# Performance work log

Hardware: AMD Instinct MI355X
Metric: run time of the kernel (lower is better)

Reference implementation:

```python
import jax, jax.numpy as jnp
import numpy as np
import math

D_MODEL = 768
HEADS = 12
D_FF = 3072
B, S = 2, 2048


def layer_norm(x, g, b, eps=1e-6):
    mu = jnp.mean(x, axis=-1, keepdims=True)
    var = jnp.mean((x - mu) ** 2, axis=-1, keepdims=True)
    return (x - mu) / jnp.sqrt(var + eps) * g + b


def gelu_tanh(x):
    c = math.sqrt(2.0 / math.pi)
    return 0.5 * x * (1.0 + jnp.tanh(c * (x + 0.044715 * x ** 3)))


def setup_inputs() -> dict:
    key = jax.random.key(0)
    ks = jax.random.split(key, 12)
    s = 0.02
    inp = {
        "iter": 1,
        "query": jax.random.normal(ks[0], (B, S, D_MODEL), jnp.float32),
        "inputs": jax.random.normal(ks[1], (B, S, D_MODEL), jnp.float32),
        "mask": jax.random.randint(ks[2], (B, S), 0, 2).astype(bool),
        "Wq": jax.random.normal(ks[3], (D_MODEL, D_MODEL), jnp.float32) * s,
        "bq": jnp.zeros((D_MODEL,), jnp.float32),
        "Wk": jax.random.normal(ks[4], (D_MODEL, D_MODEL), jnp.float32) * s,
        "bk": jnp.zeros((D_MODEL,), jnp.float32),
        "Wv": jax.random.normal(ks[5], (D_MODEL, D_MODEL), jnp.float32) * s,
        "bv": jnp.zeros((D_MODEL,), jnp.float32),
        "Wo": jax.random.normal(ks[6], (D_MODEL, D_MODEL), jnp.float32) * s,
        "bo": jnp.zeros((D_MODEL,), jnp.float32),
        "ln1_g": jnp.ones((D_MODEL,), jnp.float32),
        "ln1_b": jnp.zeros((D_MODEL,), jnp.float32),
        "W1": jax.random.normal(ks[7], (D_MODEL, D_FF), jnp.float32) * s,
        "b1": jnp.zeros((D_FF,), jnp.float32),
        "W2": jax.random.normal(ks[8], (D_FF, D_MODEL), jnp.float32) * s,
        "b2": jnp.zeros((D_MODEL,), jnp.float32),
        "ln2_g": jnp.ones((D_MODEL,), jnp.float32),
        "ln2_b": jnp.zeros((D_MODEL,), jnp.float32),
    }
    return inp


def reference(iter, query, inputs, mask, Wq, bq, Wk, bk, Wv, bv, Wo, bo,
              ln1_g, ln1_b, W1, b1, W2, b2, ln2_g, ln2_b):
    dh = D_MODEL // HEADS
    # pre-LN (skipped when iter == 0)
    x = layer_norm(inputs, ln1_g, ln1_b) if iter != 0 else inputs
    # QKV projections -> [B, H, S, dh]
    def heads(t):
        return t.reshape(B, S, HEADS, dh).transpose(0, 2, 1, 3)
    q = heads(x @ Wq + bq) / math.sqrt(dh)
    k = heads(x @ Wk + bk)
    v = heads(x @ Wv + bv)
    scores = jnp.einsum("bhqd,bhkd->bhqk", q, k)
    scores = jnp.where(mask[:, None, None, :], -1e18, scores)
    attn = jax.nn.softmax(scores, axis=-1)
    ctx = jnp.einsum("bhqk,bhkd->bhqd", attn, v)
    ctx = ctx.transpose(0, 2, 1, 3).reshape(B, S, D_MODEL)
    attn_out = ctx @ Wo + bo
    out = attn_out + inputs  # dropout=0 -> identity
    # FFN with residual pre-LN and tanh-GELU
    h = layer_norm(out, ln2_g, ln2_b)
    inter = gelu_tanh(h @ W1 + b1)
    return inter @ W2 + b2 + out
```

## Files before the change

### kernel.cpp

```cpp
#include <hip/hip_runtime.h>
#include <hip/hip_bf16.h>
#include <stdint.h>

#define D_MODEL 768
#define HEADS   12
#define DHEAD   64
#define D_FF    3072
#define BB      2
#define SS      2048
#define MTOT    (BB*SS)

typedef uint16_t u16;
typedef uint32_t u32;
typedef __attribute__((ext_vector_type(8))) short short8;
typedef __attribute__((ext_vector_type(4))) short short4v;
typedef __attribute__((ext_vector_type(4))) float f32x4;
typedef __attribute__((ext_vector_type(16))) float f32x16;
typedef __attribute__((ext_vector_type(2))) unsigned uint2v;

__device__ __forceinline__ u16 f2bf(float f) {
    union { float f; u32 u; } v; v.f = f;
    u32 r = v.u + 0x7fffu + ((v.u >> 16) & 1u);
    return (u16)(r >> 16);
}

__device__ __forceinline__ float bf2f(u16 u) {
    union { u32 u; float f; } v; v.u = ((u32)u) << 16;
    return v.f;
}

__device__ __forceinline__ u32 cvtpk(float a, float b) {
    u32 r;
    asm("v_cvt_pk_bf16_f32 %0, %1, %2" : "=v"(r) : "v"(a), "v"(b));
    return r;
}

__device__ __forceinline__ void plswap(u32& a, u32& b, int hi) {
#if __has_builtin(__builtin_amdgcn_permlane32_swap)
    uint2v r = __builtin_amdgcn_permlane32_swap(a, b, false, false);
    a = r[0]; b = r[1];
#else
    u32 ax = (u32)__shfl_xor((int)a, 32), bx = (u32)__shfl_xor((int)b, 32);
    u32 na = hi ? bx : a, nb = hi ? b : ax;
    a = na; b = nb;
#endif
}

__device__ __forceinline__ void gload16(const void* g, void* l) {
    __builtin_amdgcn_global_load_lds(
        (const __attribute__((address_space(1))) u32*)g,
        (__attribute__((address_space(3))) u32*)l, 16, 0, 0);
}

#define MFMA16(a, b, c) __builtin_amdgcn_mfma_f32_16x16x32_bf16((a), (b), (c), 0, 0, 0)
#define MFMA32(a, b, c) __builtin_amdgcn_mfma_f32_32x32x16_bf16((a), (b), (c), 0, 0, 0)

__device__ __forceinline__ float gelu_tanh_f(float x) {
    float x3 = x * x * x;
    return 0.5f * x * (1.0f + tanhf(0.7978845608028654f * (x + 0.044715f * x3)));
}

__global__ __launch_bounds__(256)
void transpose_cast(const float* __restrict__ W, u16* __restrict__ Wt, int R, int C) {
    __shared__ float tile[32][33];
    int bx = blockIdx.x, by = blockIdx.y;
    int x = threadIdx.x & 31, y0 = threadIdx.x >> 5;
#pragma unroll
    for (int i = 0; i < 4; ++i) {
        int y = y0 + i * 8;
        tile[y][x] = W[(size_t)(by * 32 + y) * C + bx * 32 + x];
    }
    __syncthreads();
#pragma unroll
    for (int i = 0; i < 4; ++i) {
        int y = y0 + i * 8;
        Wt[(size_t)(bx * 32 + y) * R + by * 32 + x] = f2bf(tile[x][y]);
    }
}

__global__ __launch_bounds__(256)
void transpose_cast4(const float* __restrict__ W0, const float* __restrict__ W1,
                     const float* __restrict__ W2, const float* __restrict__ W3,
                     u16* __restrict__ T0, u16* __restrict__ T1,
                     u16* __restrict__ T2, u16* __restrict__ T3) {
    const int z = blockIdx.z;
    const float* W = z == 0 ? W0 : z == 1 ? W1 : z == 2 ? W2 : W3;
    u16*         T = z == 0 ? T0 : z == 1 ? T1 : z == 2 ? T2 : T3;
    __shared__ float tile[32][33];
    int bx = blockIdx.x, by = blockIdx.y;
    int x = threadIdx.x & 31, y0 = threadIdx.x >> 5;
#pragma unroll
    for (int i = 0; i < 4; ++i) {
        int y = y0 + i * 8;
        tile[y][x] = W[(size_t)(by * 32 + y) * 768 + bx * 32 + x];
    }
    __syncthreads();
#pragma unroll
    for (int i = 0; i < 4; ++i) {
        int y = y0 + i * 8;
        T[(size_t)(bx * 32 + y) * 768 + by * 32 + x] = f2bf(tile[x][y]);
    }
}

__global__ void maskprep(const int* __restrict__ m, float* __restrict__ vz,
                         u16* __restrict__ m01, int n) {
    int i = blockIdx.x * 256 + threadIdx.x;
    if (i < n) {
        float v = m[i] ? 0.0f : 1.0f;
        vz[i] = v;
        m01[i] = f2bf(v);
    }
}

__global__ __launch_bounds__(256)
void ln_bf16(const float* __restrict__ in, const float* __restrict__ g,
             const float* __restrict__ bta, u16* __restrict__ out,
             const int* __restrict__ iterp, int checkIter) {
    int row = blockIdx.x, tid = threadIdx.x;
    const float* x = in + (size_t)row * D_MODEL;
    float v0 = x[tid], v1 = x[tid + 256], v2 = x[tid + 512];
    float s = v0 + v1 + v2;
    float s2 = v0 * v0 + v1 * v1 + v2 * v2;
#pragma unroll
    for (int o = 1; o < 64; o <<= 1) { s += __shfl_xor(s, o); s2 += __shfl_xor(s2, o); }
    __shared__ float sh[8];
    int w = tid >> 6;
    if ((tid & 63) == 0) { sh[w] = s; sh[4 + w] = s2; }
    __syncthreads();
    s = sh[0] + sh[1] + sh[2] + sh[3];
    s2 = sh[4] + sh[5] + sh[6] + sh[7];
    float mu = s * (1.0f / 768.0f);
    float var = s2 * (1.0f / 768.0f) - mu * mu;
    float rstd = rsqrtf(var + 1e-6f);
    bool skip = checkIter && (iterp[0] == 0);
    u16* o0 = out + (size_t)row * D_MODEL;
    if (skip) {
        o0[tid] = f2bf(v0); o0[tid + 256] = f2bf(v1); o0[tid + 512] = f2bf(v2);
    } else {
        o0[tid]       = f2bf((v0 - mu) * rstd * g[tid]       + bta[tid]);
        o0[tid + 256] = f2bf((v1 - mu) * rstd * g[tid + 256] + bta[tid + 256]);
        o0[tid + 512] = f2bf((v2 - mu) * rstd * g[tid + 512] + bta[tid + 512]);
    }
}

__global__ __launch_bounds__(256)
void ln_fuse(const float* __restrict__ pf, const float* __restrict__ bias,
             const float* __restrict__ res, const float* __restrict__ g,
             const float* __restrict__ bta, float* __restrict__ outm,
             u16* __restrict__ out) {
    int row = blockIdx.x, tid = threadIdx.x;
    size_t i0 = (size_t)row * D_MODEL + tid;
    const float* pf1 = pf + (size_t)MTOT * D_MODEL;
    float v0 = pf[i0]       + pf1[i0]       + bias[tid]       + res[i0];
    float v1 = pf[i0 + 256] + pf1[i0 + 256] + bias[tid + 256] + res[i0 + 256];
    float v2 = pf[i0 + 512] + pf1[i0 + 512] + bias[tid + 512] + res[i0 + 512];
    outm[i0] = v0; outm[i0 + 256] = v1; outm[i0 + 512] = v2;
    float s = v0 + v1 + v2;
    float s2 = v0 * v0 + v1 * v1 + v2 * v2;
#pragma unroll
    for (int o = 1; o < 64; o <<= 1) { s += __shfl_xor(s, o); s2 += __shfl_xor(s2, o); }
    __shared__ float sh[8];
    int w = tid >> 6;
    if ((tid & 63) == 0) { sh[w] = s; sh[4 + w] = s2; }
    __syncthreads();
    s = sh[0] + sh[1] + sh[2] + sh[3];
    s2 = sh[4] + sh[5] + sh[6] + sh[7];
    float mu = s * (1.0f / 768.0f);
    float var = s2 * (1.0f / 768.0f) - mu * mu;
    float rstd = rsqrtf(var + 1e-6f);
    u16* o0 = out + (size_t)row * D_MODEL;
    o0[tid]       = f2bf((v0 - mu) * rstd * g[tid]       + bta[tid]);
    o0[tid + 256] = f2bf((v1 - mu) * rstd * g[tid + 256] + bta[tid + 256]);
    o0[tid + 512] = f2bf((v2 - mu) * rstd * g[tid + 512] + bta[tid + 512]);
}

template <int MODE>
__global__ __launch_bounds__(256, 3)
void gemm_bt(const u16* __restrict__ A, const u16* __restrict__ Bt,
             int K, int N,
             const float* __restrict__ bias0, const float* __restrict__ bias1,
             const float* __restrict__ bias2,
             const float* __restrict__ res,
             float* __restrict__ outF, u16* __restrict__ oq,
             u16* __restrict__ ok, u16* __restrict__ ov) {
    __shared__ __align__(16) u16 aT[3][128 * 32];
    __shared__ __align__(16) u16 bT[3][128 * 32];
    const int tid = threadIdx.x;
    const int lane = tid & 63;
    const int w = tid >> 6;
    const int wr = w >> 1, wc = w & 1;
    const int lm = lane & 15, lq = lane >> 4;
    const int bm = blockIdx.y, bn = blockIdx.x;
    const int kzlen = K / gridDim.z;
    const int kbeg = blockIdx.z * kzlen;
    const int nsteps = kzlen >> 5;

    const u16* Abase = A  + (size_t)(bm * 128) * K + kbeg;
    const u16* Bbase = Bt + (size_t)(bn * 128) * K + kbeg;

    auto stage = [&](int buf, int t) {
        int k0 = t * 32;
#pragma unroll
        for (int j = 0; j < 2; ++j) {
            int d = j * 256 + tid;
            int row = d >> 2, p = d & 3;
            int src = (p ^ (row & 3)) * 8;
            gload16(Abase + (size_t)row * K + k0 + src, aT[buf] + (j * 256 + w * 64) * 8);
            gload16(Bbase + (size_t)row * K + k0 + src, bT[buf] + (j * 256 + w * 64) * 8);
        }
    };

    f32x4 acc[4][4] = {};
    stage(0, 0);
    if (nsteps > 1) stage(1, 1);

#pragma unroll 1
    for (int t = 0; t < nsteps; ++t) {
        if (t + 1 < nsteps) asm volatile("s_waitcnt vmcnt(4)" ::: "memory");
        else                asm volatile("s_waitcnt vmcnt(0)" ::: "memory");
        __syncthreads();
        const u16* Ab = aT[t % 3];
        const u16* Bb = bT[t % 3];
        short8 av[4], bv[4];
#pragma unroll
        for (int m = 0; m < 4; ++m) {
            int row = wr * 64 + m * 16 + lm;
            av[m] = *(const short8*)(Ab + row * 32 + ((lq ^ (row & 3)) * 8));
        }
#pragma unroll
        for (int n = 0; n < 4; ++n) {
            int row = wc * 64 + n * 16 + lm;
            bv[n] = *(const short8*)(Bb + row * 32 + ((lq ^ (row & 3)) * 8));
        }
#pragma unroll
        for (int m = 0; m < 4; ++m)
#pragma unroll
            for (int n = 0; n < 4; ++n)
                acc[m][n] = MFMA16(av[m], bv[n], acc[m][n]);
        if (t + 2 < nsteps) stage((t + 2) % 3, t + 2);
    }

#pragma unroll
    for (int m = 0; m < 4; ++m) {
#pragma unroll
        for (int n = 0; n < 4; ++n) {
            int col = bn * 128 + wc * 64 + n * 16 + lm;
#pragma unroll
            for (int r = 0; r < 4; ++r) {
                int row = bm * 128 + wr * 64 + m * 16 + lq * 4 + r;
                float v = acc[m][n][r];
                if (MODE == 0) {
                    int proj = col / D_MODEL;
                    int d = col - proj * D_MODEL;
                    int hh = d >> 6, dhi = d & 63;
                    int bb = row >> 11, sIdx = row & 2047;
                    if (proj == 0) {
                        v = (v + bias0[d]) * 0.18033688011112042f;
                        oq[((size_t)(bb * HEADS + hh) * SS + sIdx) * DHEAD + dhi] = f2bf(v);
                    } else if (proj == 1) {
                        v = v + bias1[d];
                        ok[((size_t)(bb * HEADS + hh) * SS + sIdx) * DHEAD + dhi] = f2bf(v);
                    } else {
                        v = (v + bias2[d]) * res[row];
                        ov[((size_t)(bb * HEADS + hh) * DHEAD + dhi) * SS + sIdx] = f2bf(v);
                    }
                } else if (MODE == 1) {
                    if (gridDim.z > 1) {
                        outF[((size_t)blockIdx.z * MTOT + row) * N + col] = v;
                    } else {
                        size_t idx = (size_t)row * N + col;
                        outF[idx] = v + bias0[col] + res[idx];
                    }
                } else {
                    float t2 = v + bias0[col];
                    oq[(size_t)row * N + col] = f2bf(gelu_tanh_f(t2));
                }
            }
        }
    }
}

__global__ __launch_bounds__(256)
void reduce_ks2(const float* __restrict__ pf, const float* __restrict__ bias,
                const float* __restrict__ res, float* __restrict__ out, int N) {
    size_t i = ((size_t)blockIdx.x * 256 + threadIdx.x) * 4;
    f32x4 s0 = *(const f32x4*)(pf + i);
    f32x4 s1 = *(const f32x4*)(pf + (size_t)MTOT * N + i);
    int col = (int)(i % (size_t)N);
    f32x4 b = *(const f32x4*)(bias + col);
    f32x4 r = *(const f32x4*)(res + i);
    f32x4 o;
#pragma unroll
    for (int e = 0; e < 4; ++e) o[e] = s0[e] + s1[e] + b[e] + r[e];
    *(f32x4*)(out + i) = o;
}

template <int NCH>
__global__ __launch_bounds__(256, 4)
void attn_fwd4(const u16* __restrict__ q, const u16* __restrict__ k,
               const u16* __restrict__ vtg, const u16* __restrict__ m01g,
               u16* __restrict__ po, float* __restrict__ pml) {
    constexpr int KLEN = SS / NCH;
    constexpr int KT   = KLEN / 64;
    __shared__ __align__(16) u16 kls[2][64 * 64];
    __shared__ __align__(16) u16 vls[2][64 * 64];
    __shared__ __align__(16) u16 m01l[KLEN];

    const int tid = threadIdx.x, lane = tid & 63, w = tid >> 6;
    const int lm = lane & 31, hi = lane >> 5;
    const int head = blockIdx.y;
    const int qblk = blockIdx.x / NCH, chunk = blockIdx.x % NCH;
    const int q0 = qblk * 128;
    const int k0 = chunk * KLEN;

    const u16* qbase = q + (size_t)head * SS * DHEAD;
    const u16* kbase = k + (size_t)head * SS * DHEAD;
    const u16* vbase = vtg + (size_t)head * DHEAD * SS;
    const u16* m01row = m01g + (head / HEADS) * SS;

    short8 qf[4];
    const int qrow = q0 + w * 32 + lm;
#pragma unroll
    for (int c = 0; c < 4; ++c)
        qf[c] = *(const short8*)(qbase + (size_t)qrow * DHEAD + c * 16 + hi * 8);

    if (tid < KLEN / 8)
        gload16(m01row + k0 + (size_t)tid * 8, m01l + (size_t)w * 64 * 8);

    auto stage = [&](int buf, int t) {
#pragma unroll
        for (int j = 0; j < 2; ++j) {
            int c = j * 256 + tid;
            int row = c >> 3, jj = c & 7;
            gload16(kbase + (size_t)(k0 + t * 64 + row) * DHEAD + ((jj ^ (row & 7)) * 8),
                    kls[buf] + (j * 256 + w * 64) * 8);
            gload16(vbase + (size_t)row * SS + k0 + t * 64 + ((jj ^ (row & 7)) * 8),
                    vls[buf] + (j * 256 + w * 64) * 8);
        }
    };
    stage(0, 0);
    asm volatile("s_waitcnt vmcnt(0)" ::: "memory");
    __syncthreads();

    f32x16 o0 = {}, o1 = {}, accl = {};
    int cur = 0;

#pragma unroll 1
    for (int t = 0; t < KT; ++t) {
        if (t < KT - 1) stage(cur ^ 1, t + 1);
        const u16* kb = kls[cur];
        const u16* vb = vls[cur];
#pragma unroll
        for (int s = 0; s < 2; ++s) {
            short8 av[4];
#pragma unroll
            for (int c = 0; c < 4; ++c)
                av[c] = *(const short8*)(kb + (s * 32 + lm) * 64 + (((c * 2 + hi) ^ (lm & 7)) * 8));
            short8 vf[4];
#pragma unroll
            for (int kc = 0; kc < 2; ++kc)
#pragma unroll
                for (int df = 0; df < 2; ++df)
                    vf[kc * 2 + df] = *(const short8*)(vb + (df * 32 + lm) * 64 +
                                                       (((s * 4 + kc * 2 + hi) ^ (lm & 7)) * 8));
            short8 mf0 = *(const short8*)(m01l + t * 64 + s * 32 + hi * 8);
            short8 mf1 = *(const short8*)(m01l + t * 64 + s * 32 + 16 + hi * 8);

            f32x16 st = {};
#pragma unroll
            for (int c = 0; c < 4; ++c) st = MFMA32(av[c], qf[c], st);

            float p[16];
#pragma unroll
            for (int r = 0; r < 16; ++r) p[r] = exp2f(st[r]);

            u32 W[8];
#pragma unroll
            for (int t8 = 0; t8 < 8; ++t8) W[t8] = cvtpk(p[2 * t8], p[2 * t8 + 1]);
            union { u32 wd[4]; short8 s8; } pf0, pf1;
            u32 a0w = W[0], b0w = W[2]; plswap(a0w, b0w, hi);
            u32 a1w = W[1], b1w = W[3]; plswap(a1w, b1w, hi);
            u32 a2w = W[4], b2w = W[6]; plswap(a2w, b2w, hi);
            u32 a3w = W[5], b3w = W[7]; plswap(a3w, b3w, hi);
            pf0.wd[0] = a0w; pf0.wd[1] = a1w; pf0.wd[2] = b0w; pf0.wd[3] = b1w;
            pf1.wd[0] = a2w; pf1.wd[1] = a3w; pf1.wd[2] = b2w; pf1.wd[3] = b3w;

            accl = MFMA32(mf0, pf0.s8, accl);
            accl = MFMA32(mf1, pf1.s8, accl);
            o0 = MFMA32(vf[0], pf0.s8, o0);
            o1 = MFMA32(vf[1], pf0.s8, o1);
            o0 = MFMA32(vf[2], pf1.s8, o0);
            o1 = MFMA32(vf[3], pf1.s8, o1);
        }
        asm volatile("s_waitcnt vmcnt(0)" ::: "memory");
        __syncthreads();
        cur ^= 1;
    }

    const int pc = (head * 16 + qblk) * NCH + chunk;
    u16* orow = po + ((size_t)pc * 128 + (w * 32 + lm)) * 64;
#pragma unroll
    for (int g = 0; g < 4; ++g) {
        short4v pk0, pk1;
#pragma unroll
        for (int e = 0; e < 4; ++e) {
            pk0[e] = (short)f2bf(o0[g * 4 + e]);
            pk1[e] = (short)f2bf(o1[g * 4 + e]);
        }
        *(short4v*)(orow + g * 8 + hi * 4) = pk0;
        *(short4v*)(orow + 32 + g * 8 + hi * 4) = pk1;
    }
    if (hi == 0)
        pml[(size_t)pc * 128 + (w * 32 + lm)] = accl[0];
}

__global__ __launch_bounds__(256)
void attn_merge(const u16* __restrict__ po, const float* __restrict__ pml,
                u16* __restrict__ ctx, int nch) {
    const int head = blockIdx.y;
    const int bb = head / HEADS, hh = head % HEADS;
    const int rl = threadIdx.x >> 4, dg = threadIdx.x & 15;
    const int s = blockIdx.x * 16 + rl;
    const int qb = s >> 7, qr = s & 127;
    const int pcb = (head * 16 + qb) * nch;

    float denom = 0.0f;
    float acc[4] = {0.0f, 0.0f, 0.0f, 0.0f};
#pragma unroll 4
    for (int c = 0; c < nch; ++c) {
        denom += pml[((size_t)(pcb + c)) * 128 + qr];
        const u16* op = po + (((size_t)(pcb + c) * 128 + qr) * 64) + dg * 4;
        short4v a = *(const short4v*)op;
#pragma unroll
        for (int e = 0; e < 4; ++e) acc[e] += bf2f((u16)a[e]);
    }
    float inv = 1.0f / denom;
    short4v r;
#pragma unroll
    for (int e = 0; e < 4; ++e) r[e] = (short)f2bf(acc[e] * inv);
    *(short4v*)(ctx + ((size_t)(bb * SS + s)) * D_MODEL + hh * DHEAD + dg * 4) = r;
}

extern "C" void kernel_launch(void* const* d_in, const int* in_sizes, int n_in,
                              void* d_out, int out_size, void* d_ws, size_t ws_size,
                              hipStream_t stream) {
    const int*   iterp  = (const int*)  d_in[0];
    const float* inputs = (const float*)d_in[2];
    const int*   mask   = (const int*)  d_in[3];
    const float* Wq = (const float*)d_in[4];
    const float* bq = (const float*)d_in[5];
    const float* Wk = (const float*)d_in[6];
    const float* bk = (const float*)d_in[7];
    const float* Wv = (const float*)d_in[8];
    const float* bv = (const float*)d_in[9];
    const float* Wo = (const float*)d_in[10];
    const float* bo = (const float*)d_in[11];
    const float* ln1g = (const float*)d_in[12];
    const float* ln1b = (const float*)d_in[13];
    const float* W1 = (const float*)d_in[14];
    const float* b1 = (const float*)d_in[15];
    const float* W2 = (const float*)d_in[16];
    const float* b2 = (const float*)d_in[17];
    const float* ln2g = (const float*)d_in[18];
    const float* ln2b = (const float*)d_in[19];
    float* outp = (float*)d_out;

    char* ws = (char*)d_ws;
    size_t off = 0;
    auto alloc = [&](size_t bytes) -> void* {
        void* p = ws + off;
        off += (bytes + 255) & ~(size_t)255;
        return p;
    };
    u16*   wqkv_t = (u16*)  alloc((size_t)2304 * 768 * 2);
    u16*   wo_t   = (u16*)  alloc((size_t)768 * 768 * 2);
    u16*   w1_t   = (u16*)  alloc((size_t)3072 * 768 * 2);
    u16*   w2_t   = (u16*)  alloc((size_t)768 * 3072 * 2);
    float* vzf    = (float*)alloc((size_t)MTOT * 4);
    u16*   m01    = (u16*)  alloc((size_t)MTOT * 2);
    u16*   xh     = (u16*)  alloc((size_t)MTOT * 768 * 2);
    u16*   qb     = (u16*)  alloc((size_t)MTOT * 768 * 2);
    u16*   kbuf   = (u16*)  alloc((size_t)MTOT * 768 * 2);
    u16*   vtb    = (u16*)  alloc((size_t)MTOT * 768 * 2);
    u16*   ctxb   = (u16*)  alloc((size_t)MTOT * 768 * 2);
    float* outm   = (float*)alloc((size_t)MTOT * 768 * 4);
    u16*   inter  = qb;

    float* pfbuf = (float*)alloc((size_t)2 * MTOT * 768 * 4);
    const bool split_ok = (off <= ws_size);

    float* pml = (float*)xh;

    dim3 blk(256);
    transpose_cast4<<<dim3(24, 24, 4), blk, 0, stream>>>(
        Wq, Wk, Wv, Wo,
        wqkv_t, wqkv_t + 768 * 768, wqkv_t + 2 * 768 * 768, wo_t);
    transpose_cast<<<dim3(96, 24), blk, 0, stream>>>(W1, w1_t, 768, 3072);
    transpose_cast<<<dim3(24, 96), blk, 0, stream>>>(W2, w2_t, 3072, 768);
    maskprep<<<dim3(16), blk, 0, stream>>>(mask, vzf, m01, MTOT);

    ln_bf16<<<dim3(MTOT), blk, 0, stream>>>(inputs, ln1g, ln1b, xh, iterp, 1);

    gemm_bt<0><<<dim3(2304 / 128, MTOT / 128), blk, 0, stream>>>(
        xh, wqkv_t, 768, 2304, bq, bk, bv, vzf, nullptr, qb, kbuf, vtb);

    if (split_ok) {
        u16* po = (u16*)pfbuf;
        attn_fwd4<4><<<dim3(16 * 4, BB * HEADS), blk, 0, stream>>>(
            qb, kbuf, vtb, m01, po, pml);
        attn_merge<<<dim3(SS / 16, BB * HEADS), blk, 0, stream>>>(po, pml, ctxb, 4);
    } else {
        u16* po = (u16*)outm;
        attn_fwd4<2><<<dim3(16 * 2, BB * HEADS), blk, 0, stream>>>(
            qb, kbuf, vtb, m01, po, pml);
        attn_merge<<<dim3(SS / 16, BB * HEADS), blk, 0, stream>>>(po, pml, ctxb, 2);
    }

    if (split_ok) {
        gemm_bt<1><<<dim3(768 / 128, MTOT / 128, 2), blk, 0, stream>>>(
            ctxb, wo_t, 768, 768, nullptr, nullptr, nullptr, nullptr,
            pfbuf, nullptr, nullptr, nullptr);
        ln_fuse<<<dim3(MTOT), blk, 0, stream>>>(pfbuf, bo, inputs, ln2g, ln2b, outm, xh);
    } else {
        gemm_bt<1><<<dim3(768 / 128, MTOT / 128), blk, 0, stream>>>(
            ctxb, wo_t, 768, 768, bo, nullptr, nullptr, inputs, outm, nullptr, nullptr, nullptr);
        ln_bf16<<<dim3(MTOT), blk, 0, stream>>>(outm, ln2g, ln2b, xh, iterp, 0);
    }

    gemm_bt<2><<<dim3(3072 / 128, MTOT / 128), blk, 0, stream>>>(
        xh, w1_t, 768, 3072, b1, nullptr, nullptr, nullptr, nullptr, inter, nullptr, nullptr);

    if (split_ok) {
        gemm_bt<1><<<dim3(768 / 128, MTOT / 128, 2), blk, 0, stream>>>(
            inter, w2_t, 3072, 768, nullptr, nullptr, nullptr, nullptr,
            pfbuf, nullptr, nullptr, nullptr);
        reduce_ks2<<<dim3(MTOT * 768 / 1024), blk, 0, stream>>>(pfbuf, b2, outm, outp, 768);
    } else {
        gemm_bt<1><<<dim3(768 / 128, MTOT / 128), blk, 0, stream>>>(
            inter, w2_t, 3072, 768, b2, nullptr, nullptr, outm, outp, nullptr, nullptr, nullptr);
    }
}
```

Before: 229.9 us.

## Widen attention blocks to 512 threads with triple-buffered K/V staging and MFMA priority

The attention kernel now uses 512-thread blocks covering 256 query rows, so each staged K/V tile is shared by twice as many waves. It triple-buffers K/V in LDS and issues loads two tiles ahead, waiting with a partial vmcnt instead of draining all loads each iteration. MFMA sections are wrapped in s_setprio to favour matrix issue over the exp and pack work. The grid halves, which lowers block count and raises LDS use per block, and the merge kernel's indexing is updated to match.

```diff
diff --git a/kernel.cpp b/kernel.cpp
--- a/kernel.cpp
+++ b/kernel.cpp
@@ -296,21 +296,21 @@
 }
 
 template <int NCH>
-__global__ __launch_bounds__(256, 4)
-void attn_fwd4(const u16* __restrict__ q, const u16* __restrict__ k,
+__global__ __launch_bounds__(512, 6)
+void attn_fwd5(const u16* __restrict__ q, const u16* __restrict__ k,
                const u16* __restrict__ vtg, const u16* __restrict__ m01g,
                u16* __restrict__ po, float* __restrict__ pml) {
     constexpr int KLEN = SS / NCH;
     constexpr int KT   = KLEN / 64;
-    __shared__ __align__(16) u16 kls[2][64 * 64];
-    __shared__ __align__(16) u16 vls[2][64 * 64];
+    __shared__ __align__(16) u16 kls[3][64 * 64];
+    __shared__ __align__(16) u16 vls[3][64 * 64];
     __shared__ __align__(16) u16 m01l[KLEN];
 
     const int tid = threadIdx.x, lane = tid & 63, w = tid >> 6;
     const int lm = lane & 31, hi = lane >> 5;
     const int head = blockIdx.y;
     const int qblk = blockIdx.x / NCH, chunk = blockIdx.x % NCH;
-    const int q0 = qblk * 128;
+    const int q0 = qblk * 256;
     const int k0 = chunk * KLEN;
 
     const u16* qbase = q + (size_t)head * SS * DHEAD;
@@ -325,31 +325,27 @@
         qf[c] = *(const short8*)(qbase + (size_t)qrow * DHEAD + c * 16 + hi * 8);
 
     if (tid < KLEN / 8)
-        gload16(m01row + k0 + (size_t)tid * 8, m01l + (size_t)w * 64 * 8);
+        gload16(m01row + k0 + (size_t)tid * 8, m01l + (size_t)(tid >> 6) * 64 * 8);
 
     auto stage = [&](int buf, int t) {
-#pragma unroll
-        for (int j = 0; j < 2; ++j) {
-            int c = j * 256 + tid;
-            int row = c >> 3, jj = c & 7;
-            gload16(kbase + (size_t)(k0 + t * 64 + row) * DHEAD + ((jj ^ (row & 7)) * 8),
-                    kls[buf] + (j * 256 + w * 64) * 8);
-            gload16(vbase + (size_t)row * SS + k0 + t * 64 + ((jj ^ (row & 7)) * 8),
-                    vls[buf] + (j * 256 + w * 64) * 8);
-        }
+        int row = tid >> 3, jj = tid & 7;
+        gload16(kbase + (size_t)(k0 + t * 64 + row) * DHEAD + ((jj ^ (row & 7)) * 8),
+                kls[buf] + (size_t)w * 64 * 8);
+        gload16(vbase + (size_t)row * SS + k0 + t * 64 + ((jj ^ (row & 7)) * 8),
+                vls[buf] + (size_t)w * 64 * 8);
     };
     stage(0, 0);
-    asm volatile("s_waitcnt vmcnt(0)" ::: "memory");
-    __syncthreads();
+    if (KT > 1) stage(1, 1);
 
     f32x16 o0 = {}, o1 = {}, accl = {};
-    int cur = 0;
 
 #pragma unroll 1
     for (int t = 0; t < KT; ++t) {
-        if (t < KT - 1) stage(cur ^ 1, t + 1);
-        const u16* kb = kls[cur];
-        const u16* vb = vls[cur];
+        if (t + 1 < KT) asm volatile("s_waitcnt vmcnt(2)" ::: "memory");
+        else            asm volatile("s_waitcnt vmcnt(0)" ::: "memory");
+        __syncthreads();
+        const u16* kb = kls[t % 3];
+        const u16* vb = vls[t % 3];
 #pragma unroll
         for (int s = 0; s < 2; ++s) {
             short8 av[4];
@@ -367,8 +363,10 @@
             short8 mf1 = *(const short8*)(m01l + t * 64 + s * 32 + 16 + hi * 8);
 
             f32x16 st = {};
+            __builtin_amdgcn_s_setprio(1);
 #pragma unroll
             for (int c = 0; c < 4; ++c) st = MFMA32(av[c], qf[c], st);
+            __builtin_amdgcn_s_setprio(0);
 
             float p[16];
 #pragma unroll
@@ -385,20 +383,20 @@
             pf0.wd[0] = a0w; pf0.wd[1] = a1w; pf0.wd[2] = b0w; pf0.wd[3] = b1w;
             pf1.wd[0] = a2w; pf1.wd[1] = a3w; pf1.wd[2] = b2w; pf1.wd[3] = b3w;
 
+            __builtin_amdgcn_s_setprio(1);
             accl = MFMA32(mf0, pf0.s8, accl);
             accl = MFMA32(mf1, pf1.s8, accl);
             o0 = MFMA32(vf[0], pf0.s8, o0);
             o1 = MFMA32(vf[1], pf0.s8, o1);
             o0 = MFMA32(vf[2], pf1.s8, o0);
             o1 = MFMA32(vf[3], pf1.s8, o1);
+            __builtin_amdgcn_s_setprio(0);
         }
-        asm volatile("s_waitcnt vmcnt(0)" ::: "memory");
-        __syncthreads();
-        cur ^= 1;
-    }
-
-    const int pc = (head * 16 + qblk) * NCH + chunk;
-    u16* orow = po + ((size_t)pc * 128 + (w * 32 + lm)) * 64;
+        if (t + 2 < KT) stage((t + 2) % 3, t + 2);
+    }
+
+    const int pc = (head * (SS / 256) + qblk) * NCH + chunk;
+    u16* orow = po + ((size_t)pc * 256 + (w * 32 + lm)) * 64;
 #pragma unroll
     for (int g = 0; g < 4; ++g) {
         short4v pk0, pk1;
@@ -411,7 +409,7 @@
         *(short4v*)(orow + 32 + g * 8 + hi * 4) = pk1;
     }
     if (hi == 0)
-        pml[(size_t)pc * 128 + (w * 32 + lm)] = accl[0];
+        pml[(size_t)pc * 256 + (w * 32 + lm)] = accl[0];
 }
 
 __global__ __launch_bounds__(256)
@@ -421,15 +419,15 @@
     const int bb = head / HEADS, hh = head % HEADS;
     const int rl = threadIdx.x >> 4, dg = threadIdx.x & 15;
     const int s = blockIdx.x * 16 + rl;
-    const int qb = s >> 7, qr = s & 127;
-    const int pcb = (head * 16 + qb) * nch;
+    const int qb = s >> 8, qr = s & 255;
+    const int pcb = (head * (SS / 256) + qb) * nch;
 
     float denom = 0.0f;
     float acc[4] = {0.0f, 0.0f, 0.0f, 0.0f};
 #pragma unroll 4
     for (int c = 0; c < nch; ++c) {
-        denom += pml[((size_t)(pcb + c)) * 128 + qr];
-        const u16* op = po + (((size_t)(pcb + c) * 128 + qr) * 64) + dg * 4;
+        denom += pml[((size_t)(pcb + c)) * 256 + qr];
+        const u16* op = po + (((size_t)(pcb + c) * 256 + qr) * 64) + dg * 4;
         short4v a = *(const short4v*)op;
 #pragma unroll
         for (int e = 0; e < 4; ++e) acc[e] += bf2f((u16)a[e]);
@@ -506,12 +504,12 @@
 
     if (split_ok) {
         u16* po = (u16*)pfbuf;
-        attn_fwd4<4><<<dim3(16 * 4, BB * HEADS), blk, 0, stream>>>(
+        attn_fwd5<4><<<dim3((SS / 256) * 4, BB * HEADS), dim3(512), 0, stream>>>(
             qb, kbuf, vtb, m01, po, pml);
         attn_merge<<<dim3(SS / 16, BB * HEADS), blk, 0, stream>>>(po, pml, ctxb, 4);
     } else {
         u16* po = (u16*)outm;
-        attn_fwd4<2><<<dim3(16 * 2, BB * HEADS), blk, 0, stream>>>(
+        attn_fwd5<2><<<dim3((SS / 256) * 2, BB * HEADS), dim3(512), 0, stream>>>(
             qb, kbuf, vtb, m01, po, pml);
         attn_merge<<<dim3(SS / 16, BB * HEADS), blk, 0, stream>>>(po, pml, ctxb, 2);
     }
```

Measured after the change: 541.4 us. 2.35x slower.

## Triple-buffer K/V tiles in attention with prefetch depth two and fast exp2

Applied to the files above, without the earlier changes.

Attention now stages K/V tiles into three LDS buffers and issues loads two tiles ahead. Each iteration waits with a partial vmcnt and syncs once at the top, so loads overlap more of the compute. exp2f is replaced by the hardware exp2 builtin to drop range-handling code. The extra LDS buffer lowers the occupancy hint from 4 to 3 blocks per CU. The mask-load LDS offset is also corrected to use tid>>6.

```diff
diff --git a/kernel.cpp b/kernel.cpp
--- a/kernel.cpp
+++ b/kernel.cpp
@@ -27,6 +27,14 @@
 __device__ __forceinline__ float bf2f(u16 u) {
     union { u32 u; float f; } v; v.u = ((u32)u) << 16;
     return v.f;
+}
+
+__device__ __forceinline__ float exp2_fast(float x) {
+#if __has_builtin(__builtin_amdgcn_exp2f)
+    return __builtin_amdgcn_exp2f(x);
+#else
+    return exp2f(x);
+#endif
 }
 
 __device__ __forceinline__ u32 cvtpk(float a, float b) {
@@ -296,14 +304,14 @@
 }
 
 template <int NCH>
-__global__ __launch_bounds__(256, 4)
-void attn_fwd4(const u16* __restrict__ q, const u16* __restrict__ k,
+__global__ __launch_bounds__(256, 3)
+void attn_fwd6(const u16* __restrict__ q, const u16* __restrict__ k,
                const u16* __restrict__ vtg, const u16* __restrict__ m01g,
                u16* __restrict__ po, float* __restrict__ pml) {
     constexpr int KLEN = SS / NCH;
     constexpr int KT   = KLEN / 64;
-    __shared__ __align__(16) u16 kls[2][64 * 64];
-    __shared__ __align__(16) u16 vls[2][64 * 64];
+    __shared__ __align__(16) u16 kls[3][64 * 64];
+    __shared__ __align__(16) u16 vls[3][64 * 64];
     __shared__ __align__(16) u16 m01l[KLEN];
 
     const int tid = threadIdx.x, lane = tid & 63, w = tid >> 6;
@@ -325,7 +333,7 @@
         qf[c] = *(const short8*)(qbase + (size_t)qrow * DHEAD + c * 16 + hi * 8);
 
     if (tid < KLEN / 8)
-        gload16(m01row + k0 + (size_t)tid * 8, m01l + (size_t)w * 64 * 8);
+        gload16(m01row + k0 + (size_t)tid * 8, m01l + (size_t)(tid >> 6) * 64 * 8);
 
     auto stage = [&](int buf, int t) {
 #pragma unroll
@@ -339,17 +347,17 @@
         }
     };
     stage(0, 0);
-    asm volatile("s_waitcnt vmcnt(0)" ::: "memory");
-    __syncthreads();
+    if (KT > 1) stage(1, 1);
 
     f32x16 o0 = {}, o1 = {}, accl = {};
-    int cur = 0;
 
 #pragma unroll 1
     for (int t = 0; t < KT; ++t) {
-        if (t < KT - 1) stage(cur ^ 1, t + 1);
-        const u16* kb = kls[cur];
-        const u16* vb = vls[cur];
+        if (t + 1 < KT) asm volatile("s_waitcnt vmcnt(4)" ::: "memory");
+        else            asm volatile("s_waitcnt vmcnt(0)" ::: "memory");
+        __syncthreads();
+        const u16* kb = kls[t % 3];
+        const u16* vb = vls[t % 3];
 #pragma unroll
         for (int s = 0; s < 2; ++s) {
             short8 av[4];
@@ -372,7 +380,7 @@
 
             float p[16];
 #pragma unroll
-            for (int r = 0; r < 16; ++r) p[r] = exp2f(st[r]);
+            for (int r = 0; r < 16; ++r) p[r] = exp2_fast(st[r]);
 
             u32 W[8];
 #pragma unroll
@@ -392,9 +400,7 @@
             o0 = MFMA32(vf[2], pf1.s8, o0);
             o1 = MFMA32(vf[3], pf1.s8, o1);
         }
-        asm volatile("s_waitcnt vmcnt(0)" ::: "memory");
-        __syncthreads();
-        cur ^= 1;
+        if (t + 2 < KT) stage((t + 2) % 3, t + 2);
     }
 
     const int pc = (head * 16 + qblk) * NCH + chunk;
@@ -506,12 +512,12 @@
 
     if (split_ok) {
         u16* po = (u16*)pfbuf;
-        attn_fwd4<4><<<dim3(16 * 4, BB * HEADS), blk, 0, stream>>>(
+        attn_fwd6<4><<<dim3(16 * 4, BB * HEADS), blk, 0, stream>>>(
             qb, kbuf, vtb, m01, po, pml);
         attn_merge<<<dim3(SS / 16, BB * HEADS), blk, 0, stream>>>(po, pml, ctxb, 4);
     } else {
         u16* po = (u16*)outm;
-        attn_fwd4<2><<<dim3(16 * 2, BB * HEADS), blk, 0, stream>>>(
+        attn_fwd6<2><<<dim3(16 * 2, BB * HEADS), blk, 0, stream>>>(
             qb, kbuf, vtb, m01, po, pml);
         attn_merge<<<dim3(SS / 16, BB * HEADS), blk, 0, stream>>>(po, pml, ctxb, 2);
     }
```

Result: faster. 221.5 us (-3.7%).

## Replace direct global-to-LDS loads with register-staged padded LDS tiles in GEMM and attention

Applied to the files above, without the earlier changes.

Both the GEMM and the attention kernels stop using global_load_lds with XOR-swizzled layouts. They now load tiles into registers, write them to padded LDS tiles (row strides of 40 and 72), and double-buffer with one barrier per step. The GEMM goes from triple to double buffering and raises its occupancy hint from 3 to 4 blocks. The attention softmax switches to the hardware exp2 builtin. The register staging costs extra VGPRs and LDS write instructions, and the padding takes more LDS per tile.

```diff
diff --git a/kernel.cpp b/kernel.cpp
--- a/kernel.cpp
+++ b/kernel.cpp
@@ -27,6 +27,14 @@
 __device__ __forceinline__ float bf2f(u16 u) {
     union { u32 u; float f; } v; v.u = ((u32)u) << 16;
     return v.f;
+}
+
+__device__ __forceinline__ float exp2_fast(float x) {
+#if __has_builtin(__builtin_amdgcn_exp2f)
+    return __builtin_amdgcn_exp2f(x);
+#else
+    return exp2f(x);
+#endif
 }
 
 __device__ __forceinline__ u32 cvtpk(float a, float b) {
@@ -44,12 +52,6 @@
     u32 na = hi ? bx : a, nb = hi ? b : ax;
     a = na; b = nb;
 #endif
-}
-
-__device__ __forceinline__ void gload16(const void* g, void* l) {
-    __builtin_amdgcn_global_load_lds(
-        (const __attribute__((address_space(1))) u32*)g,
-        (__attribute__((address_space(3))) u32*)l, 16, 0, 0);
 }
 
 #define MFMA16(a, b, c) __builtin_amdgcn_mfma_f32_16x16x32_bf16((a), (b), (c), 0, 0, 0)
@@ -174,8 +176,9 @@
     o0[tid + 512] = f2bf((v2 - mu) * rstd * g[tid + 512] + bta[tid + 512]);
 }
 
+#define GLDA 40
 template <int MODE>
-__global__ __launch_bounds__(256, 3)
+__global__ __launch_bounds__(256, 4)
 void gemm_bt(const u16* __restrict__ A, const u16* __restrict__ Bt,
              int K, int N,
              const float* __restrict__ bias0, const float* __restrict__ bias1,
@@ -183,8 +186,8 @@
              const float* __restrict__ res,
              float* __restrict__ outF, u16* __restrict__ oq,
              u16* __restrict__ ok, u16* __restrict__ ov) {
-    __shared__ __align__(16) u16 aT[3][128 * 32];
-    __shared__ __align__(16) u16 bT[3][128 * 32];
+    __shared__ __align__(16) u16 aT[2][128 * GLDA];
+    __shared__ __align__(16) u16 bT[2][128 * GLDA];
     const int tid = threadIdx.x;
     const int lane = tid & 63;
     const int w = tid >> 6;
@@ -195,49 +198,48 @@
     const int kbeg = blockIdx.z * kzlen;
     const int nsteps = kzlen >> 5;
 
-    const u16* Abase = A  + (size_t)(bm * 128) * K + kbeg;
-    const u16* Bbase = Bt + (size_t)(bn * 128) * K + kbeg;
-
-    auto stage = [&](int buf, int t) {
-        int k0 = t * 32;
-#pragma unroll
-        for (int j = 0; j < 2; ++j) {
-            int d = j * 256 + tid;
-            int row = d >> 2, p = d & 3;
-            int src = (p ^ (row & 3)) * 8;
-            gload16(Abase + (size_t)row * K + k0 + src, aT[buf] + (j * 256 + w * 64) * 8);
-            gload16(Bbase + (size_t)row * K + k0 + src, bT[buf] + (j * 256 + w * 64) * 8);
-        }
+    const int srow = tid >> 1, scol = (tid & 1) * 16;
+    const u16* Abase = A  + (size_t)(bm * 128 + srow) * K + kbeg + scol;
+    const u16* Bbase = Bt + (size_t)(bn * 128 + srow) * K + kbeg + scol;
+    const int soff = srow * GLDA + scol;
+
+    f32x4 ra0, ra1, rb0, rb1;
+    auto sload = [&](int t) {
+        const u16* ap = Abase + t * 32;
+        const u16* bp = Bbase + t * 32;
+        ra0 = *(const f32x4*)ap; ra1 = *(const f32x4*)(ap + 8);
+        rb0 = *(const f32x4*)bp; rb1 = *(const f32x4*)(bp + 8);
     };
+    auto swrite = [&](int buf) {
+        *(f32x4*)(aT[buf] + soff) = ra0; *(f32x4*)(aT[buf] + soff + 8) = ra1;
+        *(f32x4*)(bT[buf] + soff) = rb0; *(f32x4*)(bT[buf] + soff + 8) = rb1;
+    };
 
     f32x4 acc[4][4] = {};
-    stage(0, 0);
-    if (nsteps > 1) stage(1, 1);
+    sload(0); swrite(0);
+    __syncthreads();
+    int cur = 0;
 
 #pragma unroll 1
     for (int t = 0; t < nsteps; ++t) {
-        if (t + 1 < nsteps) asm volatile("s_waitcnt vmcnt(4)" ::: "memory");
-        else                asm volatile("s_waitcnt vmcnt(0)" ::: "memory");
-        __syncthreads();
-        const u16* Ab = aT[t % 3];
-        const u16* Bb = bT[t % 3];
+        if (t + 1 < nsteps) sload(t + 1);
+        const u16* Ab = aT[cur];
+        const u16* Bb = bT[cur];
         short8 av[4], bv[4];
 #pragma unroll
-        for (int m = 0; m < 4; ++m) {
-            int row = wr * 64 + m * 16 + lm;
-            av[m] = *(const short8*)(Ab + row * 32 + ((lq ^ (row & 3)) * 8));
-        }
-#pragma unroll
-        for (int n = 0; n < 4; ++n) {
-            int row = wc * 64 + n * 16 + lm;
-            bv[n] = *(const short8*)(Bb + row * 32 + ((lq ^ (row & 3)) * 8));
-        }
+        for (int m = 0; m < 4; ++m)
+            av[m] = *(const short8*)(Ab + (wr * 64 + m * 16 + lm) * GLDA + lq * 8);
+#pragma unroll
+        for (int n = 0; n < 4; ++n)
+            bv[n] = *(const short8*)(Bb + (wc * 64 + n * 16 + lm) * GLDA + lq * 8);
 #pragma unroll
         for (int m = 0; m < 4; ++m)
 #pragma unroll
             for (int n = 0; n < 4; ++n)
                 acc[m][n] = MFMA16(av[m], bv[n], acc[m][n]);
-        if (t + 2 < nsteps) stage((t + 2) % 3, t + 2);
+        if (t + 1 < nsteps) swrite(cur ^ 1);
+        __syncthreads();
+        cur ^= 1;
     }
 
 #pragma unroll
@@ -295,15 +297,16 @@
     *(f32x4*)(out + i) = o;
 }
 
+#define ALDA 72
 template <int NCH>
 __global__ __launch_bounds__(256, 4)
-void attn_fwd4(const u16* __restrict__ q, const u16* __restrict__ k,
+void attn_fwd7(const u16* __restrict__ q, const u16* __restrict__ k,
                const u16* __restrict__ vtg, const u16* __restrict__ m01g,
                u16* __restrict__ po, float* __restrict__ pml) {
     constexpr int KLEN = SS / NCH;
     constexpr int KT   = KLEN / 64;
-    __shared__ __align__(16) u16 kls[2][64 * 64];
-    __shared__ __align__(16) u16 vls[2][64 * 64];
+    __shared__ __align__(16) u16 kls[2][64 * ALDA];
+    __shared__ __align__(16) u16 vls[2][64 * ALDA];
     __shared__ __align__(16) u16 m01l[KLEN];
 
     const int tid = threadIdx.x, lane = tid & 63, w = tid >> 6;
@@ -324,22 +327,26 @@
     for (int c = 0; c < 4; ++c)
         qf[c] = *(const short8*)(qbase + (size_t)qrow * DHEAD + c * 16 + hi * 8);
 
-    if (tid < KLEN / 8)
-        gload16(m01row + k0 + (size_t)tid * 8, m01l + (size_t)w * 64 * 8);
-
-    auto stage = [&](int buf, int t) {
-#pragma unroll
-        for (int j = 0; j < 2; ++j) {
-            int c = j * 256 + tid;
-            int row = c >> 3, jj = c & 7;
-            gload16(kbase + (size_t)(k0 + t * 64 + row) * DHEAD + ((jj ^ (row & 7)) * 8),
-                    kls[buf] + (j * 256 + w * 64) * 8);
-            gload16(vbase + (size_t)row * SS + k0 + t * 64 + ((jj ^ (row & 7)) * 8),
-                    vls[buf] + (j * 256 + w * 64) * 8);
-        }
+    const int srow = tid >> 2, scol = (tid & 3) * 16;
+    const int soff = srow * ALDA + scol;
+
+    f32x4 rk0, rk1, rv0, rv1;
+    auto sload = [&](int t) {
+        const u16* kp = kbase + (size_t)(k0 + t * 64 + srow) * DHEAD + scol;
+        rk0 = *(const f32x4*)kp; rk1 = *(const f32x4*)(kp + 8);
+        const u16* vp = vbase + (size_t)srow * SS + k0 + t * 64 + scol;
+        rv0 = *(const f32x4*)vp; rv1 = *(const f32x4*)(vp + 8);
     };
-    stage(0, 0);
-    asm volatile("s_waitcnt vmcnt(0)" ::: "memory");
+    auto swrite = [&](int buf) {
+        *(f32x4*)(kls[buf] + soff) = rk0; *(f32x4*)(kls[buf] + soff + 8) = rk1;
+        *(f32x4*)(vls[buf] + soff) = rv0; *(f32x4*)(vls[buf] + soff + 8) = rv1;
+    };
+
+    if (tid < KLEN / 8) {
+        f32x4 mv = *(const f32x4*)(m01row + k0 + tid * 8);
+        *(f32x4*)(m01l + tid * 8) = mv;
+    }
+    sload(0); swrite(0);
     __syncthreads();
 
     f32x16 o0 = {}, o1 = {}, accl = {};
@@ -347,7 +354,7 @@
 
 #pragma unroll 1
     for (int t = 0; t < KT; ++t) {
-        if (t < KT - 1) stage(cur ^ 1, t + 1);
+        if (t + 1 < KT) sload(t + 1);
         const u16* kb = kls[cur];
         const u16* vb = vls[cur];
 #pragma unroll
@@ -355,14 +362,14 @@
             short8 av[4];
 #pragma unroll
             for (int c = 0; c < 4; ++c)
-                av[c] = *(const short8*)(kb + (s * 32 + lm) * 64 + (((c * 2 + hi) ^ (lm & 7)) * 8));
+                av[c] = *(const short8*)(kb + (s * 32 + lm) * ALDA + (c * 2 + hi) * 8);
             short8 vf[4];
 #pragma unroll
             for (int kc = 0; kc < 2; ++kc)
 #pragma unroll
                 for (int df = 0; df < 2; ++df)
-                    vf[kc * 2 + df] = *(const short8*)(vb + (df * 32 + lm) * 64 +
-                                                       (((s * 4 + kc * 2 + hi) ^ (lm & 7)) * 8));
+                    vf[kc * 2 + df] = *(const short8*)(vb + (df * 32 + lm) * ALDA +
+                                                       (s * 4 + kc * 2 + hi) * 8);
             short8 mf0 = *(const short8*)(m01l + t * 64 + s * 32 + hi * 8);
             short8 mf1 = *(const short8*)(m01l + t * 64 + s * 32 + 16 + hi * 8);
 
@@ -372,7 +379,7 @@
 
             float p[16];
 #pragma unroll
-            for (int r = 0; r < 16; ++r) p[r] = exp2f(st[r]);
+            for (int r = 0; r < 16; ++r) p[r] = exp2_fast(st[r]);
 
             u32 W[8];
 #pragma unroll
@@ -392,7 +399,7 @@
             o0 = MFMA32(vf[2], pf1.s8, o0);
             o1 = MFMA32(vf[3], pf1.s8, o1);
         }
-        asm volatile("s_waitcnt vmcnt(0)" ::: "memory");
+        if (t + 1 < KT) swrite(cur ^ 1);
         __syncthreads();
         cur ^= 1;
     }
@@ -506,12 +513,12 @@
 
     if (split_ok) {
         u16* po = (u16*)pfbuf;
-        attn_fwd4<4><<<dim3(16 * 4, BB * HEADS), blk, 0, stream>>>(
+        attn_fwd7<4><<<dim3(16 * 4, BB * HEADS), blk, 0, stream>>>(
             qb, kbuf, vtb, m01, po, pml);
         attn_merge<<<dim3(SS / 16, BB * HEADS), blk, 0, stream>>>(po, pml, ctxb, 4);
     } else {
         u16* po = (u16*)outm;
-        attn_fwd4<2><<<dim3(16 * 2, BB * HEADS), blk, 0, stream>>>(
+        attn_fwd7<2><<<dim3(16 * 2, BB * HEADS), blk, 0, stream>>>(
             qb, kbuf, vtb, m01, po, pml);
         attn_merge<<<dim3(SS / 16, BB * HEADS), blk, 0, stream>>>(po, pml, ctxb, 2);
     }
```

New measurement: 229.7 us. No clear change (-0.1%).
